# Kernel optimization log

Measured on AMD Instinct MI355X. Metric: run time of the kernel, lower is better.

Reference implementation:

```python
import jax, jax.numpy as jnp
import numpy as np

KS = 3        # kernel_size
DIL = 2       # dilation
HEAD_DIM = 32


def _unfold(x, ks, dil):
    """torch nn.Unfold(ks, dilation=dil, padding=dil*(ks-1)//2, stride=1).
    x: [B, C, H, W] -> [B, C, ks*ks, H, W] (channel-major patch order, matching torch)."""
    B, C, H, W = x.shape
    pad = dil * (ks - 1) // 2
    xp = jnp.pad(x, ((0, 0), (0, 0), (pad, pad), (pad, pad)))
    pats = [xp[:, :, i * dil:i * dil + H, j * dil:j * dil + W]
            for i in range(ks) for j in range(ks)]
    return jnp.stack(pats, axis=2)


def setup_inputs() -> dict:
    key = jax.random.key(0)
    k1, k2, k3 = jax.random.split(key, 3)
    shape = (16, 128, 64, 64)  # [B, d, H, W]
    return {
        "q": jax.random.normal(k1, shape, dtype=jnp.float32),
        "k": jax.random.normal(k2, shape, dtype=jnp.float32),
        "v": jax.random.normal(k3, shape, dtype=jnp.float32),
    }


def reference(q, k, v):
    B, d, H, W = q.shape
    heads = d // HEAD_DIM
    scale = HEAD_DIM ** (-0.5)
    KK = KS * KS
    # q: [B, heads, head_dim, H*W]
    qr = q.reshape(B, heads, HEAD_DIM, H * W)
    # unfolded k/v: [B, heads, head_dim, KK, H*W]
    ku = _unfold(k, KS, DIL).reshape(B, heads, HEAD_DIM, KK, H * W)
    vu = _unfold(v, KS, DIL).reshape(B, heads, HEAD_DIM, KK, H * W)
    # per-pixel small attention over KK local dilated keys
    attn = jnp.einsum('bhdn,bhdkn->bhnk', qr, ku) * scale  # [B,heads,HW,KK]
    attn = jax.nn.softmax(attn, axis=-1)  # attn_drop = 0 -> identity
    out = jnp.einsum('bhnk,bhdkn->bnhd', attn, vu)  # [B,HW,heads,head_dim]
    return out.reshape(B, H, W, d)
```

## Files before the change

### kernel.cpp

```cpp
#include <hip/hip_runtime.h>

namespace {
constexpr float SCALE = 0.17677669529663687f;
constexpr int CHP = 192;

typedef const __attribute__((address_space(1))) void gbl_v;
typedef __attribute__((address_space(3))) void lds_v;

__global__ __launch_bounds__(256, 3) void dilate_attn(
    const float* __restrict__ q, const float* __restrict__ k,
    const float* __restrict__ v, float* __restrict__ out) {
  __shared__ float kbuf[32 * CHP];
  __shared__ float vbuf[32 * CHP];

  const int tid = threadIdx.x;
  const int cg  = tid & 7;
  const int pp  = tid >> 3;

  const int blk   = blockIdx.x;
  const int s     = blk >> 3;
  const int combo = ((blk & 7) << 3) | (s >> 6);
  const int h     = s & 63;
  const int b     = combo >> 2;
  const int head  = combo & 3;

  const size_t cb = ((size_t)b * 128 + head * 32) * 4096;
  const float* kp = k + cb;
  const float* vp = v + cb;

  int rows[3]; float rowm[3];
  #pragma unroll
  for (int r = 0; r < 3; ++r) {
    const int ry = h + 2 * (r - 1);
    const bool ok = (unsigned)ry < 64u;
    rows[r] = (ok ? ry : h) * 64;
    rowm[r] = ok ? 1.0f : 0.0f;
  }

  const int px0 = pp << 1;
  float2 q2[4];
  #pragma unroll
  for (int ci = 0; ci < 4; ++ci) {
    q2[ci] = *(const float2*)(q + cb + (cg * 4 + ci) * 4096 + h * 64 + px0);
    q2[ci].x *= SCALE;
    q2[ci].y *= SCALE;
  }

  #pragma unroll
  for (int t = 0; t < 6; ++t) {
    const int l4  = t * 256 + tid;
    const int ch  = l4 / 48;
    const int rem = l4 - ch * 48;
    const int r   = rem >> 4;
    const int q4  = rem & 15;
    const int pxs = ((q4 - (ch >> 2)) & 15) << 2;
    const int go  = ch * 4096 + rows[r] + pxs;
    const int lo  = l4 << 2;
    __builtin_amdgcn_global_load_lds((gbl_v*)(kp + go), (lds_v*)(kbuf + lo), 16, 0, 0);
    __builtin_amdgcn_global_load_lds((gbl_v*)(vp + go), (lds_v*)(vbuf + lo), 16, 0, 0);
  }

  __syncthreads();

  const int   txL = (pp == 0)  ? 0  : px0 - 2;
  const int   txC = px0;
  const int   txR = (pp == 31) ? 62 : px0 + 2;
  const float mL  = (pp == 0)  ? 0.0f : 1.0f;
  const float mR  = (pp == 31) ? 0.0f : 1.0f;

  const int rot = cg << 2;
  const int tL  = (txL + rot) & 63;
  const int tC  = (txC + rot) & 63;
  const int tR  = (txR + rot) & 63;

  float l0[9], l1[9];
  #pragma unroll
  for (int t = 0; t < 9; ++t) { l0[t] = 0.0f; l1[t] = 0.0f; }

  #pragma unroll
  for (int r = 0; r < 3; ++r) {
    #pragma unroll
    for (int ci = 0; ci < 4; ++ci) {
      const float* kc = kbuf + (cg * 4 + ci) * CHP + r * 64;
      const float2 kL = *(const float2*)(kc + tL);
      const float2 kC = *(const float2*)(kc + tC);
      const float2 kR = *(const float2*)(kc + tR);
      const float2 qq = q2[ci];
      l0[r*3+0] = fmaf(qq.x, kL.x, l0[r*3+0]);
      l1[r*3+0] = fmaf(qq.y, kL.y, l1[r*3+0]);
      l0[r*3+1] = fmaf(qq.x, kC.x, l0[r*3+1]);
      l1[r*3+1] = fmaf(qq.y, kC.y, l1[r*3+1]);
      l0[r*3+2] = fmaf(qq.x, kR.x, l0[r*3+2]);
      l1[r*3+2] = fmaf(qq.y, kR.y, l1[r*3+2]);
    }
  }

  #pragma unroll
  for (int m = 1; m <= 4; m <<= 1) {
    #pragma unroll
    for (int t = 0; t < 9; ++t) {
      l0[t] += __shfl_xor(l0[t], m, 64);
      l1[t] += __shfl_xor(l1[t], m, 64);
    }
  }

  float msk[9];
  #pragma unroll
  for (int r = 0; r < 3; ++r) {
    msk[r*3+0] = rowm[r] * mL;
    msk[r*3+1] = rowm[r];
    msk[r*3+2] = rowm[r] * mR;
  }
  float mx0 = -1e30f, mx1 = -1e30f;
  #pragma unroll
  for (int t = 0; t < 9; ++t) {
    l0[t] *= msk[t]; l1[t] *= msk[t];
    mx0 = fmaxf(mx0, l0[t]); mx1 = fmaxf(mx1, l1[t]);
  }
  float s0 = 0.0f, s1 = 0.0f;
  #pragma unroll
  for (int t = 0; t < 9; ++t) {
    l0[t] = __expf(l0[t] - mx0);
    l1[t] = __expf(l1[t] - mx1);
    s0 += l0[t]; s1 += l1[t];
  }
  const float r0 = 1.0f / s0, r1 = 1.0f / s1;
  #pragma unroll
  for (int t = 0; t < 9; ++t) {
    l0[t] *= r0 * msk[t];
    l1[t] *= r1 * msk[t];
  }

  float o0[4] = {0, 0, 0, 0}, o1[4] = {0, 0, 0, 0};
  #pragma unroll
  for (int r = 0; r < 3; ++r) {
    #pragma unroll
    for (int ci = 0; ci < 4; ++ci) {
      const float* vc = vbuf + (cg * 4 + ci) * CHP + r * 64;
      const float2 vL = *(const float2*)(vc + tL);
      const float2 vC = *(const float2*)(vc + tC);
      const float2 vR = *(const float2*)(vc + tR);
      o0[ci] = fmaf(l0[r*3+0], vL.x, o0[ci]);
      o0[ci] = fmaf(l0[r*3+1], vC.x, o0[ci]);
      o0[ci] = fmaf(l0[r*3+2], vR.x, o0[ci]);
      o1[ci] = fmaf(l1[r*3+0], vL.y, o1[ci]);
      o1[ci] = fmaf(l1[r*3+1], vC.y, o1[ci]);
      o1[ci] = fmaf(l1[r*3+2], vR.y, o1[ci]);
    }
  }

  float* ob = out + ((size_t)(b * 64 + h) * 64 + px0) * 128 + head * 32 + cg * 4;
  *(float4*)(ob)       = make_float4(o0[0], o0[1], o0[2], o0[3]);
  *(float4*)(ob + 128) = make_float4(o1[0], o1[1], o1[2], o1[3]);
}
}

extern "C" void kernel_launch(void* const* d_in, const int* in_sizes, int n_in,
                              void* d_out, int out_size, void* d_ws, size_t ws_size,
                              hipStream_t stream) {
  const float* q = (const float*)d_in[0];
  const float* k = (const float*)d_in[1];
  const float* v = (const float*)d_in[2];
  float* o = (float*)d_out;
  dilate_attn<<<dim3(4096), dim3(256), 0, stream>>>(q, k, v, o);
}
```

Measured before the change: 143.0 us.

## Process two query rows per block sharing staged K/V rows; drop softmax max

Each 512-thread block now handles two query rows, r0 and r0+2. Both rows share four staged K/V rows in LDS, where before each row staged three of its own. This cuts the global-to-LDS traffic per output row and halves the grid size. The softmax also drops the max-subtraction pass and exponentiates the masked logits directly, which saves instructions but can overflow if logits grow large. LDS per block grows to 64KB, which limits how many blocks can be resident at once.

```diff
diff --git a/kernel.cpp b/kernel.cpp
--- a/kernel.cpp
+++ b/kernel.cpp
@@ -2,12 +2,12 @@
 
 namespace {
 constexpr float SCALE = 0.17677669529663687f;
-constexpr int CHP = 192;
+constexpr int CHP = 256;
 
 typedef const __attribute__((address_space(1))) void gbl_v;
 typedef __attribute__((address_space(3))) void lds_v;
 
-__global__ __launch_bounds__(256, 3) void dilate_attn(
+__global__ __launch_bounds__(512, 4) void dilate_attn(
     const float* __restrict__ q, const float* __restrict__ k,
     const float* __restrict__ v, float* __restrict__ out) {
   __shared__ float kbuf[32 * CHP];
@@ -15,46 +15,49 @@
 
   const int tid = threadIdx.x;
   const int cg  = tid & 7;
-  const int pp  = tid >> 3;
+  const int pp  = (tid >> 3) & 31;
+  const int rg  = tid >> 8;
 
   const int blk   = blockIdx.x;
   const int s     = blk >> 3;
-  const int combo = ((blk & 7) << 3) | (s >> 6);
-  const int h     = s & 63;
+  const int combo = ((blk & 7) << 3) | (s >> 5);
+  const int pr    = s & 31;
+  const int r0    = ((pr >> 1) << 2) | (pr & 1);
   const int b     = combo >> 2;
   const int head  = combo & 3;
+  const int qrow  = r0 + 2 * rg;
 
   const size_t cb = ((size_t)b * 128 + head * 32) * 4096;
   const float* kp = k + cb;
   const float* vp = v + cb;
 
-  int rows[3]; float rowm[3];
+  int srow[4]; float vm[4];
   #pragma unroll
-  for (int r = 0; r < 3; ++r) {
-    const int ry = h + 2 * (r - 1);
+  for (int j = 0; j < 4; ++j) {
+    const int ry = r0 - 2 + 2 * j;
     const bool ok = (unsigned)ry < 64u;
-    rows[r] = (ok ? ry : h) * 64;
-    rowm[r] = ok ? 1.0f : 0.0f;
+    srow[j] = (ok ? ry : r0) * 64;
+    vm[j]   = ok ? 1.0f : 0.0f;
   }
 
   const int px0 = pp << 1;
   float2 q2[4];
   #pragma unroll
   for (int ci = 0; ci < 4; ++ci) {
-    q2[ci] = *(const float2*)(q + cb + (cg * 4 + ci) * 4096 + h * 64 + px0);
+    q2[ci] = *(const float2*)(q + cb + (cg * 4 + ci) * 4096 + qrow * 64 + px0);
     q2[ci].x *= SCALE;
     q2[ci].y *= SCALE;
   }
 
   #pragma unroll
-  for (int t = 0; t < 6; ++t) {
-    const int l4  = t * 256 + tid;
-    const int ch  = l4 / 48;
-    const int rem = l4 - ch * 48;
+  for (int t = 0; t < 4; ++t) {
+    const int l4  = t * 512 + tid;
+    const int ch  = l4 >> 6;
+    const int rem = l4 & 63;
     const int r   = rem >> 4;
     const int q4  = rem & 15;
     const int pxs = ((q4 - (ch >> 2)) & 15) << 2;
-    const int go  = ch * 4096 + rows[r] + pxs;
+    const int go  = ch * 4096 + srow[r] + pxs;
     const int lo  = l4 << 2;
     __builtin_amdgcn_global_load_lds((gbl_v*)(kp + go), (lds_v*)(kbuf + lo), 16, 0, 0);
     __builtin_amdgcn_global_load_lds((gbl_v*)(vp + go), (lds_v*)(vbuf + lo), 16, 0, 0);
@@ -73,6 +76,8 @@
   const int tC  = (txC + rot) & 63;
   const int tR  = (txR + rot) & 63;
 
+  const int rbase = rg;
+
   float l0[9], l1[9];
   #pragma unroll
   for (int t = 0; t < 9; ++t) { l0[t] = 0.0f; l1[t] = 0.0f; }
@@ -81,7 +86,7 @@
   for (int r = 0; r < 3; ++r) {
     #pragma unroll
     for (int ci = 0; ci < 4; ++ci) {
-      const float* kc = kbuf + (cg * 4 + ci) * CHP + r * 64;
+      const float* kc = kbuf + (cg * 4 + ci) * CHP + (rbase + r) * 64;
       const float2 kL = *(const float2*)(kc + tL);
       const float2 kC = *(const float2*)(kc + tC);
       const float2 kR = *(const float2*)(kc + tR);
@@ -107,28 +112,22 @@
   float msk[9];
   #pragma unroll
   for (int r = 0; r < 3; ++r) {
-    msk[r*3+0] = rowm[r] * mL;
-    msk[r*3+1] = rowm[r];
-    msk[r*3+2] = rowm[r] * mR;
-  }
-  float mx0 = -1e30f, mx1 = -1e30f;
-  #pragma unroll
-  for (int t = 0; t < 9; ++t) {
-    l0[t] *= msk[t]; l1[t] *= msk[t];
-    mx0 = fmaxf(mx0, l0[t]); mx1 = fmaxf(mx1, l1[t]);
+    msk[r*3+0] = vm[rbase + r] * mL;
+    msk[r*3+1] = vm[rbase + r];
+    msk[r*3+2] = vm[rbase + r] * mR;
   }
   float s0 = 0.0f, s1 = 0.0f;
   #pragma unroll
   for (int t = 0; t < 9; ++t) {
-    l0[t] = __expf(l0[t] - mx0);
-    l1[t] = __expf(l1[t] - mx1);
+    l0[t] = __expf(l0[t] * msk[t]);
+    l1[t] = __expf(l1[t] * msk[t]);
     s0 += l0[t]; s1 += l1[t];
   }
-  const float r0 = 1.0f / s0, r1 = 1.0f / s1;
+  const float r0v = 1.0f / s0, r1v = 1.0f / s1;
   #pragma unroll
   for (int t = 0; t < 9; ++t) {
-    l0[t] *= r0 * msk[t];
-    l1[t] *= r1 * msk[t];
+    l0[t] *= r0v * msk[t];
+    l1[t] *= r1v * msk[t];
   }
 
   float o0[4] = {0, 0, 0, 0}, o1[4] = {0, 0, 0, 0};
@@ -136,7 +135,7 @@
   for (int r = 0; r < 3; ++r) {
     #pragma unroll
     for (int ci = 0; ci < 4; ++ci) {
-      const float* vc = vbuf + (cg * 4 + ci) * CHP + r * 64;
+      const float* vc = vbuf + (cg * 4 + ci) * CHP + (rbase + r) * 64;
       const float2 vL = *(const float2*)(vc + tL);
       const float2 vC = *(const float2*)(vc + tC);
       const float2 vR = *(const float2*)(vc + tR);
@@ -149,7 +148,7 @@
     }
   }
 
-  float* ob = out + ((size_t)(b * 64 + h) * 64 + px0) * 128 + head * 32 + cg * 4;
+  float* ob = out + ((size_t)(b * 64 + qrow) * 64 + px0) * 128 + head * 32 + cg * 4;
   *(float4*)(ob)       = make_float4(o0[0], o0[1], o0[2], o0[3]);
   *(float4*)(ob + 128) = make_float4(o1[0], o1[1], o1[2], o1[3]);
 }
@@ -162,5 +161,5 @@
   const float* k = (const float*)d_in[1];
   const float* v = (const float*)d_in[2];
   float* o = (float*)d_out;
-  dilate_attn<<<dim3(4096), dim3(256), 0, stream>>>(q, k, v, o);
+  dilate_attn<<<dim3(2048), dim3(512), 0, stream>>>(q, k, v, o);
 }
```

Result: faster. 139.4 us (-2.6%).
